# Kernel optimization log

Hardware: AMD Instinct MI355X
Metric: run time of the kernel (lower is better)

The kernel has to match this reference:

```python
import jax, jax.numpy as jnp
import numpy as np

C = 1.0           # Poincare ball curvature magnitude (k = -1/c with c=1)
MIN_NORM = 1e-15
PROJ_EPS = 4e-3   # geoopt float32 boundary eps


def _artanh(x):
    return jnp.arctanh(jnp.clip(x, -1.0 + 1e-7, 1.0 - 1e-7))


def _norm(x):
    return jnp.maximum(jnp.linalg.norm(x, axis=-1, keepdims=True), MIN_NORM)


def mobius_matvec(W, x, c=C):
    # geoopt pmath.mobius_matvec with k=-c
    sc = jnp.sqrt(c)
    x_norm = _norm(x)
    Mx = x @ W.T
    Mx_norm = _norm(Mx)
    return jnp.tanh(Mx_norm / x_norm * _artanh(sc * x_norm)) * Mx / (Mx_norm * sc)


def mobius_add(x, y, c=C):
    x2 = jnp.sum(x * x, axis=-1, keepdims=True)
    y2 = jnp.sum(y * y, axis=-1, keepdims=True)
    xy = jnp.sum(x * y, axis=-1, keepdims=True)
    num = (1.0 + 2.0 * c * xy + c * y2) * x + (1.0 - c * x2) * y
    den = 1.0 + 2.0 * c * xy + c * c * x2 * y2
    return num / jnp.maximum(den, MIN_NORM)


def project(x, c=C):
    norm = _norm(x)
    maxnorm = (1.0 - PROJ_EPS) / jnp.sqrt(c)
    return jnp.where(norm > maxnorm, x / norm * maxnorm, x)


def expmap0(u, c=C):
    sc = jnp.sqrt(c)
    un = _norm(u)
    return jnp.tanh(sc * un) * u / (sc * un)


def mobius_linear(x, W, b, c=C):
    # hyperbolic_input=True, hyperbolic_bias=True, nonlin=None
    out = mobius_matvec(W, x, c)
    out = mobius_add(out, b, c)
    return project(out, c)


def setup_inputs() -> dict:
    key = jax.random.key(0)
    ks = jax.random.split(key, 7)
    N, D = 2048, 1024        # batch*tlen, input_size
    V = 32000                # output_size (vocab)
    SLEN, B, CV = 512, 32, 500
    hidden = jax.random.normal(ks[0], (N, D), jnp.float32) * 0.1
    hidden = project(hidden)
    attn = jax.random.uniform(ks[1], (N, SLEN), jnp.float32)
    src_map = jax.random.uniform(ks[2], (SLEN, B, CV), jnp.float32)
    W = jax.random.normal(ks[3], (V, D), jnp.float32) * 0.01
    b = expmap0(jax.random.normal(ks[4], (V,), jnp.float32) / 4.0)
    Wc = jax.random.normal(ks[5], (1, D), jnp.float32) * 0.01
    bc = expmap0(jax.random.normal(ks[6], (1,), jnp.float32) / 4.0)
    return {"hidden": hidden, "attn": attn, "src_map": src_map,
            "W": W, "b": b, "Wc": Wc, "bc": bc, "pad_idx": 1}


def reference(hidden, attn, src_map, W, b, Wc, bc, pad_idx):
    slen, batch, cvocab = src_map.shape
    logits = mobius_linear(hidden, W, b)                  # (N, V)
    logits = logits.at[:, pad_idx].set(-jnp.inf)
    prob = jax.nn.softmax(logits, axis=1)
    p_copy = jax.nn.sigmoid(mobius_linear(hidden, Wc, bc))  # (N, 1)
    out_prob = prob * (1.0 - p_copy)
    mul_attn = attn * p_copy                              # (N, slen)
    a = mul_attn.reshape(-1, batch, slen)                 # (tlen, batch, slen)
    copy_prob = jnp.einsum('tbs,sbc->tbc', a, src_map).reshape(-1, cvocab)
    return jnp.concatenate([out_prob, copy_prob], axis=1)
```

## Files before the change

kernel.cpp:

```cpp
#include <hip/hip_runtime.h>
#include <stdint.h>

#define N_ROWS   2048
#define D_IN     1024
#define V_OUT    32000
#define SLEN_C   512
#define BATCH_C  32
#define CVOC     500
#define OUT_COLS 32500

#define MIN_NORM_F 1e-15f
#define PROJ_EPS_F 4e-3f

typedef __bf16 bf16x8_t __attribute__((ext_vector_type(8)));
typedef float  f32x4_t  __attribute__((ext_vector_type(4)));
typedef unsigned short ushort8_t __attribute__((ext_vector_type(8)));

__device__ __forceinline__ unsigned short f2bf(float f) {
    uint32_t b = __float_as_uint(f);
    b += 0x7FFFu + ((b >> 16) & 1u);
    return (unsigned short)(b >> 16);
}
__device__ __forceinline__ float bf2f(unsigned short u) {
    return __uint_as_float(((uint32_t)u) << 16);
}
__device__ __forceinline__ float wave_sum(float v) {
#pragma unroll
    for (int off = 32; off > 0; off >>= 1) v += __shfl_down(v, off, 64);
    return v;
}

__device__ __forceinline__ void load_lds16(const void* g, void* l) {
    __builtin_amdgcn_global_load_lds(
        (const __attribute__((address_space(1))) void*)g,
        (__attribute__((address_space(3))) void*)l, 16, 0, 0);
}

__global__ __launch_bounds__(256)
void cast_f32_to_bf16(const float* __restrict__ src, unsigned short* __restrict__ dst, int n4) {
    int i = blockIdx.x * blockDim.x + threadIdx.x;
    int stride = gridDim.x * blockDim.x;
    for (; i < n4; i += stride) {
        float4 v = ((const float4*)src)[i];
        ushort4 o;
        o.x = f2bf(v.x); o.y = f2bf(v.y); o.z = f2bf(v.z); o.w = f2bf(v.w);
        ((ushort4*)dst)[i] = o;
    }
}

__global__ __launch_bounds__(256)
void row_stats(const float* __restrict__ hidden, const float* __restrict__ Wc,
               const float* __restrict__ bc_in, float* __restrict__ g_arr,
               float* __restrict__ pc_arr) {
    __shared__ float red[8];
    const int n = blockIdx.x;
    const int tid = threadIdx.x;
    float4 hv = *(const float4*)(hidden + (size_t)n * D_IN + tid * 4);
    float4 wv = *(const float4*)(Wc + tid * 4);
    float s = hv.x * hv.x + hv.y * hv.y + hv.z * hv.z + hv.w * hv.w;
    float d = hv.x * wv.x + hv.y * wv.y + hv.z * wv.z + hv.w * wv.w;
    s = wave_sum(s); d = wave_sum(d);
    const int w = tid >> 6, l = tid & 63;
    if (l == 0) { red[w] = s; red[4 + w] = d; }
    __syncthreads();
    if (tid == 0) {
        float S  = red[0] + red[1] + red[2] + red[3];
        float Dc = red[4] + red[5] + red[6] + red[7];
        float xn = fmaxf(sqrtf(S), MIN_NORM_F);
        float xc = fminf(xn, 1.f - 1e-7f);
        float at = 0.5f * logf((1.f + xc) / (1.f - xc));
        float g = at / xn;
        float mxn = fmaxf(fabsf(Dc), MIN_NORM_F);
        float res = tanhf(mxn * g) * (Dc / mxn);
        float bcv = bc_in[0];
        float x2 = res * res, y2 = bcv * bcv, xyv = res * bcv;
        float num = (1.f + 2.f * xyv + y2) * res + (1.f - x2) * bcv;
        float dn  = fmaxf(1.f + 2.f * xyv + x2 * y2, MIN_NORM_F);
        float o = num / dn;
        float an = fmaxf(fabsf(o), MIN_NORM_F);
        float mxp = 1.f - PROJ_EPS_F;
        if (an > mxp) o = o / an * mxp;
        pc_arr[n] = 1.f / (1.f + expf(-o));
        g_arr[n]  = g;
    }
}

__global__ __launch_bounds__(256)
void gemm_bt_bf16(const unsigned short* __restrict__ A,
                  const unsigned short* __restrict__ B,
                  unsigned short* __restrict__ Cb)
{
    __shared__ unsigned short Als[128 * 64];
    __shared__ unsigned short Bls[128 * 64];
    const int tid  = threadIdx.x;
    const int wave = tid >> 6;
    const int lane = tid & 63;
    const int f   = blockIdx.x;
    const int st  = f / 400;
    const int loc = f - st * 400;
    const int am0 = (loc & 15) * 128;
    const int bn0 = (st * 25 + (loc >> 4)) * 128;

    const int srow  = lane >> 3;
    const int skoff = (lane & 7) * 8;
    const int fr = lane & 15;
    const int fk = (lane >> 4) * 8;
    const int wm = (wave >> 1) * 64;
    const int wn = (wave & 1) * 64;

    f32x4_t acc[4][4] = {};

    for (int kt = 0; kt < D_IN; kt += 64) {
#pragma unroll
        for (int q = 0; q < 4; ++q) {
            const int r0 = wave * 8 + q * 32;
            load_lds16(A + (size_t)(am0 + r0 + srow) * D_IN + kt + skoff, &Als[r0 * 64]);
            load_lds16(B + (size_t)(bn0 + r0 + srow) * D_IN + kt + skoff, &Bls[r0 * 64]);
        }
        __syncthreads();
#pragma unroll
        for (int kk = 0; kk < 64; kk += 32) {
            bf16x8_t af[4], bfr[4];
#pragma unroll
            for (int i = 0; i < 4; ++i)
                af[i] = *(const bf16x8_t*)&Als[(wm + i * 16 + fr) * 64 + kk + fk];
#pragma unroll
            for (int j = 0; j < 4; ++j)
                bfr[j] = *(const bf16x8_t*)&Bls[(wn + j * 16 + fr) * 64 + kk + fk];
#pragma unroll
            for (int i = 0; i < 4; ++i)
#pragma unroll
                for (int j = 0; j < 4; ++j)
                    acc[i][j] = __builtin_amdgcn_mfma_f32_16x16x32_bf16(af[i], bfr[j], acc[i][j], 0, 0, 0);
        }
        __syncthreads();
    }

    const int cm = (lane >> 4) * 4;
    const int cn = lane & 15;
#pragma unroll
    for (int i = 0; i < 4; ++i) {
#pragma unroll
        for (int j = 0; j < 4; ++j) {
            const int mg = am0 + wm + i * 16 + cm;
            const int ng = bn0 + wn + j * 16 + cn;
            unsigned short* cp = Cb + (size_t)mg * (OUT_COLS * 2) + ng;
#pragma unroll
            for (int r = 0; r < 4; ++r)
                cp[(size_t)r * (OUT_COLS * 2)] = f2bf(acc[i][j][r]);
        }
    }
}

__global__ __launch_bounds__(1024)
void softmax_epi(float* __restrict__ Cout, const float* __restrict__ bvec,
                 const float* __restrict__ g_arr, const float* __restrict__ pc_arr,
                 const int* __restrict__ pad_ptr) {
    __shared__ unsigned short mxls[V_OUT];
    __shared__ float red[48];
    __shared__ float bcast[4];
    const int n = blockIdx.x;
    const int tid = threadIdx.x;
    float* row = Cout + (size_t)n * OUT_COLS;
    const unsigned short* rowb = (const unsigned short*)row;
    const int pad = *pad_ptr;

    float s1 = 0.f, s2 = 0.f, s3 = 0.f;
    for (int i = tid * 8; i < V_OUT; i += 8192) {
        ushort8_t mu = *(const ushort8_t*)(rowb + i);
        float4 b0 = *(const float4*)(bvec + i);
        float4 b1 = *(const float4*)(bvec + i + 4);
        float m0 = bf2f(mu[0]), m1 = bf2f(mu[1]), m2 = bf2f(mu[2]), m3 = bf2f(mu[3]);
        float m4 = bf2f(mu[4]), m5 = bf2f(mu[5]), m6 = bf2f(mu[6]), m7 = bf2f(mu[7]);
        s1 += (m0*m0 + m1*m1 + m2*m2 + m3*m3) + (m4*m4 + m5*m5 + m6*m6 + m7*m7);
        s2 += (m0*b0.x + m1*b0.y + m2*b0.z + m3*b0.w) + (m4*b1.x + m5*b1.y + m6*b1.z + m7*b1.w);
        s3 += (b0.x*b0.x + b0.y*b0.y + b0.z*b0.z + b0.w*b0.w)
            + (b1.x*b1.x + b1.y*b1.y + b1.z*b1.z + b1.w*b1.w);
        *(ushort8_t*)&mxls[i] = mu;
    }
    s1 = wave_sum(s1); s2 = wave_sum(s2); s3 = wave_sum(s3);
    const int w = tid >> 6, l = tid & 63;
    if (l == 0) { red[w] = s1; red[16 + w] = s2; red[32 + w] = s3; }
    __syncthreads();
    if (tid == 0) {
        float S1 = 0.f, S2 = 0.f, Sb = 0.f;
        for (int k = 0; k < 16; ++k) { S1 += red[k]; S2 += red[16 + k]; Sb += red[32 + k]; }
        const float g  = g_arr[n];
        const float r   = fmaxf(sqrtf(S1), MIN_NORM_F);
        const float t   = tanhf(r * g);
        const float smv = t / r;
        const float x2 = smv * smv * S1;
        const float xy = smv * S2;
        const float den = fmaxf(1.f + 2.f * xy + x2 * Sb, MIN_NORM_F);
        float P = (1.f + 2.f * xy + Sb) * smv / den;
        float Q = (1.f - x2) / den;
        const float nrm = fmaxf(sqrtf(P * P * S1 + 2.f * P * Q * S2 + Q * Q * Sb), MIN_NORM_F);
        const float mxp = 1.f - PROJ_EPS_F;
        if (nrm > mxp) { const float fsc = mxp / nrm; P *= fsc; Q *= fsc; }
        bcast[0] = P; bcast[1] = Q;
    }
    __syncthreads();
    const float P = bcast[0], Q = bcast[1];

    float z = 0.f;
    for (int i = tid * 8; i < V_OUT; i += 8192) {
        ushort8_t mu = *(const ushort8_t*)&mxls[i];
        float4 b0 = *(const float4*)(bvec + i);
        float4 b1 = *(const float4*)(bvec + i + 4);
        float e0 = __expf(fmaf(P, bf2f(mu[0]), Q * b0.x));
        float e1 = __expf(fmaf(P, bf2f(mu[1]), Q * b0.y));
        float e2 = __expf(fmaf(P, bf2f(mu[2]), Q * b0.z));
        float e3 = __expf(fmaf(P, bf2f(mu[3]), Q * b0.w));
        float e4 = __expf(fmaf(P, bf2f(mu[4]), Q * b1.x));
        float e5 = __expf(fmaf(P, bf2f(mu[5]), Q * b1.y));
        float e6 = __expf(fmaf(P, bf2f(mu[6]), Q * b1.z));
        float e7 = __expf(fmaf(P, bf2f(mu[7]), Q * b1.w));
        if (i + 0 == pad) e0 = 0.f;
        if (i + 1 == pad) e1 = 0.f;
        if (i + 2 == pad) e2 = 0.f;
        if (i + 3 == pad) e3 = 0.f;
        if (i + 4 == pad) e4 = 0.f;
        if (i + 5 == pad) e5 = 0.f;
        if (i + 6 == pad) e6 = 0.f;
        if (i + 7 == pad) e7 = 0.f;
        z += ((e0 + e1) + (e2 + e3)) + ((e4 + e5) + (e6 + e7));
        ushort8_t eu;
        eu[0] = f2bf(e0); eu[1] = f2bf(e1); eu[2] = f2bf(e2); eu[3] = f2bf(e3);
        eu[4] = f2bf(e4); eu[5] = f2bf(e5); eu[6] = f2bf(e6); eu[7] = f2bf(e7);
        *(ushort8_t*)&mxls[i] = eu;
    }
    z = wave_sum(z);
    if (l == 0) red[w] = z;
    __syncthreads();
    if (tid == 0) {
        float a = 0.f;
        for (int k = 0; k < 16; ++k) a += red[k];
        bcast[2] = a;
    }
    __syncthreads();
    const float scale = (1.f - pc_arr[n]) / bcast[2];

    for (int i = tid * 8; i < V_OUT; i += 8192) {
        ushort8_t eu = *(const ushort8_t*)&mxls[i];
        float4 o0, o1;
        o0.x = bf2f(eu[0]) * scale; o0.y = bf2f(eu[1]) * scale;
        o0.z = bf2f(eu[2]) * scale; o0.w = bf2f(eu[3]) * scale;
        o1.x = bf2f(eu[4]) * scale; o1.y = bf2f(eu[5]) * scale;
        o1.z = bf2f(eu[6]) * scale; o1.w = bf2f(eu[7]) * scale;
        *(float4*)(row + i) = o0;
        *(float4*)(row + i + 4) = o1;
    }
}

__global__ __launch_bounds__(128)
void copy_einsum(const float* __restrict__ attn, const float* __restrict__ src_map,
                 const float* __restrict__ pc_arr, float* __restrict__ Cout) {
    __shared__ float atile[32][128];
    const int tid = threadIdx.x;
    const int cc = blockIdx.x;
    const int b  = blockIdx.y;
    const int t0 = blockIdx.z * 32;
    const int c = cc * 128 + tid;
    const bool cv = (c < CVOC);

    float acc[32];
#pragma unroll
    for (int t = 0; t < 32; ++t) acc[t] = 0.f;

    for (int s0 = 0; s0 < SLEN_C; s0 += 128) {
        __syncthreads();
        for (int idx = tid; idx < 32 * 128; idx += 128) {
            const int t = idx >> 7, s = idx & 127;
            atile[t][s] = attn[(size_t)((t0 + t) * BATCH_C + b) * SLEN_C + s0 + s];
        }
        __syncthreads();
        for (int j = 0; j < 128; j += 4) {
            float sv0 = 0.f, sv1 = 0.f, sv2 = 0.f, sv3 = 0.f;
            if (cv) {
                const float* sp = src_map + (size_t)(s0 + j) * (BATCH_C * CVOC) + b * CVOC + c;
                sv0 = sp[0];
                sv1 = sp[BATCH_C * CVOC];
                sv2 = sp[2 * BATCH_C * CVOC];
                sv3 = sp[3 * BATCH_C * CVOC];
            }
#pragma unroll
            for (int t = 0; t < 32; ++t) {
                const float4 av = *(const float4*)&atile[t][j];
                acc[t] = fmaf(av.x, sv0, acc[t]);
                acc[t] = fmaf(av.y, sv1, acc[t]);
                acc[t] = fmaf(av.z, sv2, acc[t]);
                acc[t] = fmaf(av.w, sv3, acc[t]);
            }
        }
    }
    if (cv) {
#pragma unroll
        for (int t = 0; t < 32; ++t) {
            const int n = (t0 + t) * BATCH_C + b;
            Cout[(size_t)n * OUT_COLS + V_OUT + c] = acc[t] * pc_arr[n];
        }
    }
}

extern "C" void kernel_launch(void* const* d_in, const int* in_sizes, int n_in,
                              void* d_out, int out_size, void* d_ws, size_t ws_size,
                              hipStream_t stream) {
    const float* hidden  = (const float*)d_in[0];
    const float* attn    = (const float*)d_in[1];
    const float* src_map = (const float*)d_in[2];
    const float* W       = (const float*)d_in[3];
    const float* bvec    = (const float*)d_in[4];
    const float* Wc      = (const float*)d_in[5];
    const float* bc      = (const float*)d_in[6];
    const int*   padp    = (const int*)d_in[7];
    float* out = (float*)d_out;

    const int wb_elems = V_OUT * D_IN;
    const int hb_elems = N_ROWS * D_IN;
    unsigned short* Wb = (unsigned short*)d_ws;
    unsigned short* Hb = Wb + wb_elems;
    float* g_arr  = (float*)(Hb + hb_elems);
    float* pc_arr = g_arr + N_ROWS;

    cast_f32_to_bf16<<<4000, 256, 0, stream>>>(W, Wb, wb_elems / 4);
    cast_f32_to_bf16<<<512, 256, 0, stream>>>(hidden, Hb, hb_elems / 4);
    row_stats<<<N_ROWS, 256, 0, stream>>>(hidden, Wc, bc, g_arr, pc_arr);

    gemm_bt_bf16<<<4000, 256, 0, stream>>>(Hb, Wb, (unsigned short*)out);

    softmax_epi<<<N_ROWS, 1024, 0, stream>>>(out, bvec, g_arr, pc_arr, padp);

    dim3 egrid(4, BATCH_C, 2);
    copy_einsum<<<egrid, 128, 0, stream>>>(attn, src_map, pc_arr, out);
}
```

Measured before the change: 799.6 us.

## Rewrite bf16 GEMM as 256x256 tile with double-buffered LDS pipeline

Replaces the 128x128 single-buffered GEMM with a 256x256 tile computed by 8 waves. LDS is double-buffered, and global loads for the next K slice are interleaved with MFMA groups under explicit vmcnt waits and barriers. LDS rows use an XOR swizzle to avoid bank conflicts, and block indices are remapped for L2 locality. The aim is to hide load latency and raise arithmetic intensity. The cost is more registers (launch bounds 512 with 2 blocks per CU), 128KB of LDS per block, and a fragile hand-written schedule.

```diff
diff --git a/kernel.cpp b/kernel.cpp
--- a/kernel.cpp
+++ b/kernel.cpp
@@ -85,69 +85,115 @@
     }
 }
 
-__global__ __launch_bounds__(256)
-void gemm_bt_bf16(const unsigned short* __restrict__ A,
-                  const unsigned short* __restrict__ B,
+
+#define STG_A(bufi, chunk, kti) \
+    load_lds16(Ag + (size_t)(am0 + ((chunk) << 6) + wave8 + srow) * D_IN + ((kti) << 6) + sk, \
+               &Asmem[bufi][(((chunk) << 6) + wave8) << 6])
+#define STG_B(bufi, chunk, kti) \
+    load_lds16(Bg + (size_t)(bn0 + ((chunk) << 6) + wave8 + srow) * D_IN + ((kti) << 6) + sk, \
+               &Bsmem[bufi][(((chunk) << 6) + wave8) << 6])
+
+#define VMCNT(N) \
+    __builtin_amdgcn_sched_barrier(0); \
+    asm volatile("s_waitcnt vmcnt(" #N ")" ::: "memory"); \
+    __builtin_amdgcn_sched_barrier(0);
+
+#define RD_A(RB, MH) \
+    _Pragma("unroll") for (int i = 0; i < 4; ++i) { \
+        const int r_ = (wm + (MH)*64 + i*16 + fr) << 6; \
+        af0[i] = *(const bf16x8_t*)&Asmem[RB][r_ + e0]; \
+        af1[i] = *(const bf16x8_t*)&Asmem[RB][r_ + e1]; }
+
+#define RD_B(RB, J0) \
+    _Pragma("unroll") for (int j = 0; j < 2; ++j) { \
+        const int r_ = (wn + ((J0) + j)*16 + fr) << 6; \
+        bf0[(J0)+j] = *(const bf16x8_t*)&Bsmem[RB][r_ + e0]; \
+        bf1[(J0)+j] = *(const bf16x8_t*)&Bsmem[RB][r_ + e1]; }
+
+#define MM(MH, J0) \
+    __builtin_amdgcn_sched_barrier(0); \
+    __builtin_amdgcn_s_barrier(); \
+    asm volatile("s_waitcnt lgkmcnt(0)" ::: "memory"); \
+    __builtin_amdgcn_sched_barrier(0); \
+    __builtin_amdgcn_s_setprio(1); \
+    _Pragma("unroll") for (int i = 0; i < 4; ++i) \
+        _Pragma("unroll") for (int j = 0; j < 2; ++j) { \
+            acc[(MH)*4+i][(J0)+j] = __builtin_amdgcn_mfma_f32_16x16x32_bf16(af0[i], bf0[(J0)+j], acc[(MH)*4+i][(J0)+j], 0, 0, 0); \
+            acc[(MH)*4+i][(J0)+j] = __builtin_amdgcn_mfma_f32_16x16x32_bf16(af1[i], bf1[(J0)+j], acc[(MH)*4+i][(J0)+j], 0, 0, 0); } \
+    __builtin_amdgcn_s_setprio(0); \
+    __builtin_amdgcn_s_barrier(); \
+    __builtin_amdgcn_sched_barrier(0);
+
+__global__ __launch_bounds__(512, 2)
+void gemm_bt_bf16(const unsigned short* __restrict__ Ag,
+                  const unsigned short* __restrict__ Bg,
                   unsigned short* __restrict__ Cb)
 {
-    __shared__ unsigned short Als[128 * 64];
-    __shared__ unsigned short Bls[128 * 64];
+    __shared__ __align__(16) unsigned short Asmem[2][256 * 64];
+    __shared__ __align__(16) unsigned short Bsmem[2][256 * 64];
     const int tid  = threadIdx.x;
     const int wave = tid >> 6;
     const int lane = tid & 63;
+
     const int f   = blockIdx.x;
-    const int st  = f / 400;
-    const int loc = f - st * 400;
-    const int am0 = (loc & 15) * 128;
-    const int bn0 = (st * 25 + (loc >> 4)) * 128;
-
+    const int swz = (f & 7) * 125 + (f >> 3);
+    const int am0 = (swz & 7) * 256;
+    const int bn0 = (swz >> 3) * 256;
+
+    const int wr = wave >> 2, wc = wave & 3;
+    const int wm = wr * 128, wn = wc * 64;
+    const int fr  = lane & 15;
+    const int fkb = (lane >> 4) << 4;
+    const int swzr = (fr & 7) << 4;
+    const int e0 = (fkb ^ swzr) >> 1;
+    const int e1 = ((64 + fkb) ^ swzr) >> 1;
+    const int wave8 = wave << 3;
     const int srow  = lane >> 3;
-    const int skoff = (lane & 7) * 8;
-    const int fr = lane & 15;
-    const int fk = (lane >> 4) * 8;
-    const int wm = (wave >> 1) * 64;
-    const int wn = (wave & 1) * 64;
-
-    f32x4_t acc[4][4] = {};
-
-    for (int kt = 0; kt < D_IN; kt += 64) {
-#pragma unroll
-        for (int q = 0; q < 4; ++q) {
-            const int r0 = wave * 8 + q * 32;
-            load_lds16(A + (size_t)(am0 + r0 + srow) * D_IN + kt + skoff, &Als[r0 * 64]);
-            load_lds16(B + (size_t)(bn0 + r0 + srow) * D_IN + kt + skoff, &Bls[r0 * 64]);
-        }
-        __syncthreads();
-#pragma unroll
-        for (int kk = 0; kk < 64; kk += 32) {
-            bf16x8_t af[4], bfr[4];
-#pragma unroll
-            for (int i = 0; i < 4; ++i)
-                af[i] = *(const bf16x8_t*)&Als[(wm + i * 16 + fr) * 64 + kk + fk];
-#pragma unroll
-            for (int j = 0; j < 4; ++j)
-                bfr[j] = *(const bf16x8_t*)&Bls[(wn + j * 16 + fr) * 64 + kk + fk];
-#pragma unroll
-            for (int i = 0; i < 4; ++i)
-#pragma unroll
-                for (int j = 0; j < 4; ++j)
-                    acc[i][j] = __builtin_amdgcn_mfma_f32_16x16x32_bf16(af[i], bfr[j], acc[i][j], 0, 0, 0);
-        }
-        __syncthreads();
-    }
-
-    const int cm = (lane >> 4) * 4;
+    const int sk    = ((lane & 7) ^ srow) << 3;
+
+    f32x4_t acc[8][4] = {};
+    bf16x8_t af0[4], af1[4], bf0[4], bf1[4];
+
+    STG_A(0, 0, 0); STG_A(0, 1, 0); STG_A(0, 2, 0); STG_A(0, 3, 0);
+    STG_B(0, 0, 0); STG_B(0, 1, 0); STG_B(0, 2, 0); STG_B(0, 3, 0);
+    STG_A(1, 0, 1); STG_A(1, 2, 1);
+    VMCNT(2)
+    __builtin_amdgcn_s_barrier();
+
+    for (int t = 0; t < 7; ++t) {
+        const int k1 = 2 * t + 1, k2 = 2 * t + 2, k3 = 2 * t + 3;
+        RD_A(0, 0); RD_B(0, 0); STG_B(1, 0, k1); STG_B(1, 1, k1); MM(0, 0);
+        RD_B(0, 2);             STG_B(1, 2, k1); STG_B(1, 3, k1); MM(0, 2);
+        RD_A(0, 1);             STG_A(1, 1, k1); STG_A(1, 3, k1); MM(1, 0);
+        STG_A(0, 0, k2); STG_A(0, 2, k2);
+        VMCNT(2)                                                  MM(1, 2);
+        RD_A(1, 0); RD_B(1, 0); STG_B(0, 0, k2); STG_B(0, 1, k2); MM(0, 0);
+        RD_B(1, 2);             STG_B(0, 2, k2); STG_B(0, 3, k2); MM(0, 2);
+        RD_A(1, 1);             STG_A(0, 1, k2); STG_A(0, 3, k2);
+                                STG_A(1, 0, k3); STG_A(1, 2, k3); MM(1, 0);
+        VMCNT(2)                                                  MM(1, 2);
+    }
+    RD_A(0, 0); RD_B(0, 0); STG_B(1, 0, 15); STG_B(1, 1, 15); MM(0, 0);
+    RD_B(0, 2);             STG_B(1, 2, 15); STG_B(1, 3, 15); MM(0, 2);
+    RD_A(0, 1);             STG_A(1, 1, 15); STG_A(1, 3, 15); MM(1, 0);
+    VMCNT(0)                                                  MM(1, 2);
+    RD_A(1, 0); RD_B(1, 0); MM(0, 0);
+    RD_B(1, 2);             MM(0, 2);
+    RD_A(1, 1);             MM(1, 0);
+                            MM(1, 2);
+
+    const int cm = (lane >> 4) << 2;
     const int cn = lane & 15;
 #pragma unroll
-    for (int i = 0; i < 4; ++i) {
-#pragma unroll
-        for (int j = 0; j < 4; ++j) {
-            const int mg = am0 + wm + i * 16 + cm;
-            const int ng = bn0 + wn + j * 16 + cn;
+    for (int I = 0; I < 8; ++I) {
+#pragma unroll
+        for (int J = 0; J < 4; ++J) {
+            const int mg = am0 + wm + I * 16 + cm;
+            const int ng = bn0 + wn + J * 16 + cn;
             unsigned short* cp = Cb + (size_t)mg * (OUT_COLS * 2) + ng;
 #pragma unroll
             for (int r = 0; r < 4; ++r)
-                cp[(size_t)r * (OUT_COLS * 2)] = f2bf(acc[i][j][r]);
+                cp[(size_t)r * (OUT_COLS * 2)] = f2bf(acc[I][J][r]);
         }
     }
 }
@@ -326,7 +372,7 @@
     cast_f32_to_bf16<<<512, 256, 0, stream>>>(hidden, Hb, hb_elems / 4);
     row_stats<<<N_ROWS, 256, 0, stream>>>(hidden, Wc, bc, g_arr, pc_arr);
 
-    gemm_bt_bf16<<<4000, 256, 0, stream>>>(Hb, Wb, (unsigned short*)out);
+    gemm_bt_bf16<<<1000, 512, 0, stream>>>(Hb, Wb, (unsigned short*)out);
 
     softmax_epi<<<N_ROWS, 1024, 0, stream>>>(out, bvec, g_arr, pc_arr, padp);
 
```

Measured after the change: 761.0 us. 4.8% less time.
